# Kernel optimization log

Measured on AMD Instinct MI355X. Metric: run time of the kernel, lower is better.

Reference implementation:

```python
import jax, jax.numpy as jnp
import numpy as np

N_U = 8192  # users (rows of adj)
N_I = 8192  # items (cols of adj)
D_IN = 2048
D_H = 2048


def setup_inputs() -> dict:
    key = jax.random.key(0)
    k1, k2, k3, k4, k5 = jax.random.split(key, 5)
    input = jax.random.normal(k1, (N_U + N_I, D_IN), dtype=jnp.float32)
    adj = jax.random.uniform(k2, (N_U, N_I), dtype=jnp.float32)
    degree = jax.random.uniform(k3, (N_U + N_I,), dtype=jnp.float32)
    # Linear params (torch Linear: y = x @ W.T + b), xavier-normal-ish init
    W = jax.random.normal(k4, (D_H, D_IN), dtype=jnp.float32) * (2.0 / (D_IN + D_H)) ** 0.5
    b = jax.random.normal(k5, (D_H,), dtype=jnp.float32) * 0.01
    return {"input": input, "adj": adj, "degree": degree, "W": W, "b": b}


def reference(input, adj, degree, W, b):
    # Original builds block adjacency B = [[0, A], [A^T, 0]], then
    # output = diag(degree) @ B @ (dropout(input) @ W^T + b).
    # dropout p=0 (eval) -> identity. We avoid materializing B: the block
    # structure means user rows aggregate item supports and vice versa.
    n_u = adj.shape[0]
    support = input @ W.T + b                      # [N_u+N_i, D_h]
    sup_u, sup_i = support[:n_u], support[n_u:]
    out_u = degree[:n_u, None] * (adj @ sup_i)     # [N_u, D_h]
    out_i = degree[n_u:, None] * (adj.T @ sup_u)   # [N_i, D_h]
    return jnp.concatenate([out_u, out_i], axis=0)
```

## Files before the change

### kernel.cpp

```cpp
#include <hip/hip_runtime.h>
#include <hip/hip_bf16.h>


typedef __bf16 bf16;
typedef bf16 bf16x4 __attribute__((ext_vector_type(4)));
typedef bf16 bf16x8 __attribute__((ext_vector_type(8)));
typedef float f32x4 __attribute__((ext_vector_type(4)));

#define AS1 __attribute__((address_space(1)))
#define AS3 __attribute__((address_space(3)))

__global__ __launch_bounds__(256) void k_cvt(const float* __restrict__ src,
                                             bf16* __restrict__ dst) {
  long i = ((long)blockIdx.x * 256 + threadIdx.x) * 4;
  float4 v = *(const float4*)(src + i);
  bf16x4 o;
  o.x = (bf16)v.x; o.y = (bf16)v.y; o.z = (bf16)v.z; o.w = (bf16)v.w;
  *(bf16x4*)(dst + i) = o;
}

__global__ __launch_bounds__(256) void k_transpose_cvt(const float* __restrict__ src,
                                                       bf16* __restrict__ dst, int n) {
  __shared__ float tile[64][65];
  const int bx = blockIdx.x * 64;
  const int by = blockIdx.y * 64;
  const int tx = threadIdx.x & 15, ty = threadIdx.x >> 4;
#pragma unroll
  for (int p = 0; p < 4; ++p) {
    float4 v = *(const float4*)(src + (long)(by + p * 16 + ty) * n + bx + tx * 4);
    tile[p * 16 + ty][tx * 4 + 0] = v.x;
    tile[p * 16 + ty][tx * 4 + 1] = v.y;
    tile[p * 16 + ty][tx * 4 + 2] = v.z;
    tile[p * 16 + ty][tx * 4 + 3] = v.w;
  }
  __syncthreads();
#pragma unroll
  for (int p = 0; p < 4; ++p) {
    bf16x4 o;
    o.x = (bf16)tile[tx * 4 + 0][p * 16 + ty];
    o.y = (bf16)tile[tx * 4 + 1][p * 16 + ty];
    o.z = (bf16)tile[tx * 4 + 2][p * 16 + ty];
    o.w = (bf16)tile[tx * 4 + 3][p * 16 + ty];
    *(bf16x4*)(dst + (long)(bx + p * 16 + ty) * n + by + tx * 4) = o;
  }
}

template <bool OUT_BF16>
__global__ __launch_bounds__(256) void k_gemm_nt(
    const bf16* __restrict__ A, const bf16* __restrict__ B, void* __restrict__ Cout,
    int K, int lda, int ldb, int ldc,
    const float* __restrict__ rowscale, const float* __restrict__ rowbias) {
  constexpr int BK = 64;
  __shared__ __align__(16) bf16 As[128 * BK];
  __shared__ __align__(16) bf16 Bs[128 * BK];
  const int tid = threadIdx.x;
  const int wave = tid >> 6, lane = tid & 63;
  const int quad = lane >> 4, l16 = lane & 15;
  const int bm = blockIdx.y * 128, bn = blockIdx.x * 128;
  const bf16* Ab = A + (long)bm * lda;
  const bf16* Bb = B + (long)bn * ldb;
  f32x4 acc[4][4] = {};
  const int mrow = (wave & 1) * 64 + l16;
  const int ncol = (wave >> 1) * 64 + l16;
  const int xm = l16 & 7;

  for (int k0 = 0; k0 < K; k0 += BK) {
    __syncthreads();
#pragma unroll
    for (int it = 0; it < 4; ++it) {
      const int c = it * 256 + tid;
      const int row = c >> 3;
      const int kc = ((c & 7) ^ (row & 7)) * 8;
      __builtin_amdgcn_global_load_lds((AS1 void*)(Ab + row * lda + k0 + kc),
                                       (AS3 void*)(As + c * 8), 16, 0, 0);
      __builtin_amdgcn_global_load_lds((AS1 void*)(Bb + row * ldb + k0 + kc),
                                       (AS3 void*)(Bs + c * 8), 16, 0, 0);
    }
    __syncthreads();
#pragma unroll
    for (int ks = 0; ks < 2; ++ks) {
      const int jl = ks * 4 + quad;
      bf16x8 af[4], bfr[4];
#pragma unroll
      for (int i = 0; i < 4; ++i)
        af[i] = *(const bf16x8*)(As + (mrow + i * 16) * BK + ((jl ^ xm) << 3));
#pragma unroll
      for (int j = 0; j < 4; ++j)
        bfr[j] = *(const bf16x8*)(Bs + (ncol + j * 16) * BK + ((jl ^ xm) << 3));
#pragma unroll
      for (int i = 0; i < 4; ++i)
#pragma unroll
        for (int j = 0; j < 4; ++j)
          acc[i][j] = __builtin_amdgcn_mfma_f32_16x16x32_bf16(af[i], bfr[j], acc[i][j], 0, 0, 0);
    }
  }

#pragma unroll
  for (int i = 0; i < 4; ++i) {
    const int r0 = bm + (wave & 1) * 64 + i * 16 + quad * 4;
    float sc[4], bi[4];
#pragma unroll
    for (int r = 0; r < 4; ++r) {
      sc[r] = rowscale ? rowscale[r0 + r] : 1.0f;
      bi[r] = rowbias ? rowbias[r0 + r] : 0.0f;
    }
#pragma unroll
    for (int j = 0; j < 4; ++j) {
      const int col = bn + (wave >> 1) * 64 + j * 16 + l16;
#pragma unroll
      for (int r = 0; r < 4; ++r) {
        float v = acc[i][j][r] * sc[r] + bi[r];
        long idx = (long)(r0 + r) * ldc + col;
        if (OUT_BF16) ((bf16*)Cout)[idx] = (bf16)v;
        else          ((float*)Cout)[idx] = v;
      }
    }
  }
}

extern "C" void kernel_launch(void* const* d_in, const int* in_sizes, int n_in,
                              void* d_out, int out_size, void* d_ws, size_t ws_size,
                              hipStream_t stream) {
  const float* input  = (const float*)d_in[0];
  const float* adj    = (const float*)d_in[1];
  const float* degree = (const float*)d_in[2];
  const float* W      = (const float*)d_in[3];
  const float* b      = (const float*)d_in[4];
  float* out = (float*)d_out;

  char* ws = (char*)d_ws;
  bf16* supT   = (bf16*)(ws);
  bf16* in_bf  = (bf16*)(ws + (64ULL  << 20));
  bf16* W_bf   = (bf16*)(ws + (128ULL << 20));
  bf16* adj_bf = (bf16*)(ws + (64ULL  << 20));
  bf16* adjT   = (bf16*)(ws + (192ULL << 20));

  k_cvt<<<(16384 * 2048 / 4) / 256, 256, 0, stream>>>(input, in_bf);
  k_cvt<<<(2048 * 2048 / 4) / 256, 256, 0, stream>>>(W, W_bf);

  k_gemm_nt<true><<<dim3(16384 / 128, 2048 / 128), 256, 0, stream>>>(
      W_bf, in_bf, supT, 2048, 2048, 2048, 16384, nullptr, b);

  k_cvt<<<(8192 * 8192 / 4) / 256, 256, 0, stream>>>(adj, adj_bf);
  k_transpose_cvt<<<dim3(128, 128), 256, 0, stream>>>(adj, adjT, 8192);

  k_gemm_nt<false><<<dim3(2048 / 128, 8192 / 128), 256, 0, stream>>>(
      adj_bf, supT + 8192, out, 8192, 8192, 16384, 2048, degree, nullptr);

  k_gemm_nt<false><<<dim3(2048 / 128, 8192 / 128), 256, 0, stream>>>(
      adjT, supT, out + 8192LL * 2048, 8192, 8192, 16384, 2048, degree + 8192, nullptr);
}
```

Baseline: 1.421 ms.

## Use 256x256 double-buffered 8-wave GEMM and fuse adj convert with transpose

Replaces the 128x128 single-buffered GEMM with a 256x256-tile, 512-thread kernel. It double-buffers LDS and splits each K-step into four MFMA phases, interleaving the next tile's global-to-LDS loads with explicit waitcnt/barrier scheduling and setprio. It also merges the adj bf16 conversion and the transpose into one kernel, so adj is read from HBM once instead of twice. The larger tiles raise arithmetic intensity and overlap loads with compute, but LDS use per block grows to 128KB and the grid gets fewer blocks, which may limit occupancy.

```diff
diff --git a/kernel.cpp b/kernel.cpp
--- a/kernel.cpp
+++ b/kernel.cpp
@@ -19,19 +19,24 @@
   *(bf16x4*)(dst + i) = o;
 }
 
-__global__ __launch_bounds__(256) void k_transpose_cvt(const float* __restrict__ src,
-                                                       bf16* __restrict__ dst, int n) {
+__global__ __launch_bounds__(256) void k_adj_cvt(const float* __restrict__ src,
+                                                 bf16* __restrict__ dst,
+                                                 bf16* __restrict__ dstT, int n) {
   __shared__ float tile[64][65];
   const int bx = blockIdx.x * 64;
   const int by = blockIdx.y * 64;
   const int tx = threadIdx.x & 15, ty = threadIdx.x >> 4;
 #pragma unroll
   for (int p = 0; p < 4; ++p) {
-    float4 v = *(const float4*)(src + (long)(by + p * 16 + ty) * n + bx + tx * 4);
+    const long r = by + p * 16 + ty;
+    float4 v = *(const float4*)(src + r * n + bx + tx * 4);
     tile[p * 16 + ty][tx * 4 + 0] = v.x;
     tile[p * 16 + ty][tx * 4 + 1] = v.y;
     tile[p * 16 + ty][tx * 4 + 2] = v.z;
     tile[p * 16 + ty][tx * 4 + 3] = v.w;
+    bf16x4 o;
+    o.x = (bf16)v.x; o.y = (bf16)v.y; o.z = (bf16)v.z; o.w = (bf16)v.w;
+    *(bf16x4*)(dst + r * n + bx + tx * 4) = o;
   }
   __syncthreads();
 #pragma unroll
@@ -41,63 +46,148 @@
     o.y = (bf16)tile[tx * 4 + 1][p * 16 + ty];
     o.z = (bf16)tile[tx * 4 + 2][p * 16 + ty];
     o.w = (bf16)tile[tx * 4 + 3][p * 16 + ty];
-    *(bf16x4*)(dst + (long)(bx + p * 16 + ty) * n + by + tx * 4) = o;
-  }
+    *(bf16x4*)(dstT + (long)(bx + p * 16 + ty) * n + by + tx * 4) = o;
+  }
+}
+
+__device__ __forceinline__ void stage_a(const bf16* Ab, bf16* lds, int lda, int k0,
+                                        int g, int tid) {
+#pragma unroll
+  for (int it = 0; it < 2; ++it) {
+    const int u = it * 512 + tid;
+    const int row = ((u >> 9) << 7) + (g << 6) + ((u >> 3) & 63);
+    const int kc = (((u & 7) ^ (row & 7)) << 3);
+    const int c = ((u >> 9) << 10) + (g << 9) + (u & 511);
+    __builtin_amdgcn_global_load_lds((const AS1 void*)(Ab + (long)row * lda + k0 + kc),
+                                     (AS3 void*)(lds + c * 8), 16, 0, 0);
+  }
+}
+
+__device__ __forceinline__ void stage_b(const bf16* Bb, bf16* lds, int ldb, int k0,
+                                        int g, int tid) {
+#pragma unroll
+  for (int it = 0; it < 2; ++it) {
+    const int u = it * 512 + tid;
+    const int r = (g << 7) + (u >> 3);
+    const int p = (((u >> 8) & 3) << 6) + (g << 5) + ((u >> 3) & 31);
+    const int kc = (((u & 7) ^ (r & 7)) << 3);
+    __builtin_amdgcn_global_load_lds((const AS1 void*)(Bb + (long)p * ldb + k0 + kc),
+                                     (AS3 void*)(lds + ((g << 10) + u) * 8), 16, 0, 0);
+  }
+}
+
+template <int MH, int NH>
+__device__ __forceinline__ void mfma_phase(f32x4 (&acc)[8][4],
+                                           const bf16x8 (&af)[4][2],
+                                           const bf16x8 (&bfr)[2][2][2]) {
+  __builtin_amdgcn_s_setprio(1);
+#pragma unroll
+  for (int i = 0; i < 4; ++i)
+#pragma unroll
+    for (int j = 0; j < 2; ++j)
+#pragma unroll
+      for (int ks = 0; ks < 2; ++ks)
+        acc[MH * 4 + i][NH * 2 + j] = __builtin_amdgcn_mfma_f32_16x16x32_bf16(
+            af[i][ks], bfr[NH][j][ks], acc[MH * 4 + i][NH * 2 + j], 0, 0, 0);
+  __builtin_amdgcn_s_setprio(0);
 }
 
 template <bool OUT_BF16>
-__global__ __launch_bounds__(256) void k_gemm_nt(
+__global__ __launch_bounds__(512, 2) void k_gemm_nt_8p(
     const bf16* __restrict__ A, const bf16* __restrict__ B, void* __restrict__ Cout,
     int K, int lda, int ldb, int ldc,
     const float* __restrict__ rowscale, const float* __restrict__ rowbias) {
-  constexpr int BK = 64;
-  __shared__ __align__(16) bf16 As[128 * BK];
-  __shared__ __align__(16) bf16 Bs[128 * BK];
+  __shared__ __align__(16) bf16 As[2][256 * 64];
+  __shared__ __align__(16) bf16 Bs[2][256 * 64];
   const int tid = threadIdx.x;
   const int wave = tid >> 6, lane = tid & 63;
   const int quad = lane >> 4, l16 = lane & 15;
-  const int bm = blockIdx.y * 128, bn = blockIdx.x * 128;
+  const int wm = wave >> 2, wn = wave & 3;
+  const int xm = l16 & 7;
+  const int bm = blockIdx.y * 256, bn = blockIdx.x * 256;
   const bf16* Ab = A + (long)bm * lda;
   const bf16* Bb = B + (long)bn * ldb;
-  f32x4 acc[4][4] = {};
-  const int mrow = (wave & 1) * 64 + l16;
-  const int ncol = (wave >> 1) * 64 + l16;
-  const int xm = l16 & 7;
-
-  for (int k0 = 0; k0 < K; k0 += BK) {
-    __syncthreads();
-#pragma unroll
-    for (int it = 0; it < 4; ++it) {
-      const int c = it * 256 + tid;
-      const int row = c >> 3;
-      const int kc = ((c & 7) ^ (row & 7)) * 8;
-      __builtin_amdgcn_global_load_lds((AS1 void*)(Ab + row * lda + k0 + kc),
-                                       (AS3 void*)(As + c * 8), 16, 0, 0);
-      __builtin_amdgcn_global_load_lds((AS1 void*)(Bb + row * ldb + k0 + kc),
-                                       (AS3 void*)(Bs + c * 8), 16, 0, 0);
-    }
-    __syncthreads();
-#pragma unroll
-    for (int ks = 0; ks < 2; ++ks) {
-      const int jl = ks * 4 + quad;
-      bf16x8 af[4], bfr[4];
-#pragma unroll
-      for (int i = 0; i < 4; ++i)
-        af[i] = *(const bf16x8*)(As + (mrow + i * 16) * BK + ((jl ^ xm) << 3));
-#pragma unroll
-      for (int j = 0; j < 4; ++j)
-        bfr[j] = *(const bf16x8*)(Bs + (ncol + j * 16) * BK + ((jl ^ xm) << 3));
-#pragma unroll
-      for (int i = 0; i < 4; ++i)
-#pragma unroll
-        for (int j = 0; j < 4; ++j)
-          acc[i][j] = __builtin_amdgcn_mfma_f32_16x16x32_bf16(af[i], bfr[j], acc[i][j], 0, 0, 0);
-    }
-  }
-
-#pragma unroll
-  for (int i = 0; i < 4; ++i) {
-    const int r0 = bm + (wave & 1) * 64 + i * 16 + quad * 4;
+
+  f32x4 acc[8][4] = {};
+  bf16x8 af[4][2], bfr[2][2][2];
+
+  stage_a(Ab, As[0], lda, 0, 0, tid);
+  stage_b(Bb, Bs[0], ldb, 0, 0, tid);
+  stage_a(Ab, As[0], lda, 0, 1, tid);
+  stage_b(Bb, Bs[0], ldb, 0, 1, tid);
+  asm volatile("s_waitcnt vmcnt(4)" ::: "memory");
+  __builtin_amdgcn_s_barrier();
+
+  const int nt = K >> 6;
+  for (int t = 0; t < nt; ++t) {
+    const int cur = t & 1, nx = cur ^ 1;
+    const int k1 = (t + 1) << 6;
+    const bool pre = (t + 1) < nt;
+    const bf16* Ac = As[cur];
+    const bf16* Bc = Bs[cur];
+
+#pragma unroll
+    for (int i = 0; i < 4; ++i)
+#pragma unroll
+      for (int ks = 0; ks < 2; ++ks)
+        af[i][ks] = *(const bf16x8*)(Ac + (wm * 128 + i * 16 + l16) * 64 +
+                                     ((((ks << 2) + quad) ^ xm) << 3));
+#pragma unroll
+    for (int j = 0; j < 2; ++j)
+#pragma unroll
+      for (int ks = 0; ks < 2; ++ks)
+        bfr[0][j][ks] = *(const bf16x8*)(Bc + (wn * 32 + j * 16 + l16) * 64 +
+                                         ((((ks << 2) + quad) ^ xm) << 3));
+    if (pre) {
+      stage_a(Ab, As[nx], lda, k1, 0, tid);
+      stage_b(Bb, Bs[nx], ldb, k1, 0, tid);
+    }
+    __builtin_amdgcn_s_barrier();
+    asm volatile("s_waitcnt lgkmcnt(0)" ::: "memory");
+    __builtin_amdgcn_sched_barrier(0);
+    mfma_phase<0, 0>(acc, af, bfr);
+    if (pre) asm volatile("s_waitcnt vmcnt(4)" ::: "memory");
+    else     asm volatile("s_waitcnt vmcnt(0)" ::: "memory");
+    __builtin_amdgcn_s_barrier();
+
+#pragma unroll
+    for (int j = 0; j < 2; ++j)
+#pragma unroll
+      for (int ks = 0; ks < 2; ++ks)
+        bfr[1][j][ks] = *(const bf16x8*)(Bc + (128 + wn * 32 + j * 16 + l16) * 64 +
+                                         ((((ks << 2) + quad) ^ xm) << 3));
+    if (pre) {
+      stage_a(Ab, As[nx], lda, k1, 1, tid);
+      stage_b(Bb, Bs[nx], ldb, k1, 1, tid);
+    }
+    __builtin_amdgcn_s_barrier();
+    asm volatile("s_waitcnt lgkmcnt(0)" ::: "memory");
+    __builtin_amdgcn_sched_barrier(0);
+    mfma_phase<0, 1>(acc, af, bfr);
+    __builtin_amdgcn_s_barrier();
+
+#pragma unroll
+    for (int i = 0; i < 4; ++i)
+#pragma unroll
+      for (int ks = 0; ks < 2; ++ks)
+        af[i][ks] = *(const bf16x8*)(Ac + (wm * 128 + 64 + i * 16 + l16) * 64 +
+                                     ((((ks << 2) + quad) ^ xm) << 3));
+    __builtin_amdgcn_s_barrier();
+    asm volatile("s_waitcnt lgkmcnt(0)" ::: "memory");
+    __builtin_amdgcn_sched_barrier(0);
+    mfma_phase<1, 0>(acc, af, bfr);
+    __builtin_amdgcn_s_barrier();
+
+    mfma_phase<1, 1>(acc, af, bfr);
+    if (pre) {
+      asm volatile("s_waitcnt vmcnt(4)" ::: "memory");
+      __builtin_amdgcn_s_barrier();
+    }
+  }
+
+#pragma unroll
+  for (int mi = 0; mi < 8; ++mi) {
+    const int r0 = bm + wm * 128 + mi * 16 + quad * 4;
     float sc[4], bi[4];
 #pragma unroll
     for (int r = 0; r < 4; ++r) {
@@ -106,10 +196,10 @@
     }
 #pragma unroll
     for (int j = 0; j < 4; ++j) {
-      const int col = bn + (wave >> 1) * 64 + j * 16 + l16;
+      const int col = bn + wn * 64 + j * 16 + l16;
 #pragma unroll
       for (int r = 0; r < 4; ++r) {
-        float v = acc[i][j][r] * sc[r] + bi[r];
+        float v = acc[mi][j][r] * sc[r] + bi[r];
         long idx = (long)(r0 + r) * ldc + col;
         if (OUT_BF16) ((bf16*)Cout)[idx] = (bf16)v;
         else          ((float*)Cout)[idx] = v;
@@ -138,15 +228,14 @@
   k_cvt<<<(16384 * 2048 / 4) / 256, 256, 0, stream>>>(input, in_bf);
   k_cvt<<<(2048 * 2048 / 4) / 256, 256, 0, stream>>>(W, W_bf);
 
-  k_gemm_nt<true><<<dim3(16384 / 128, 2048 / 128), 256, 0, stream>>>(
+  k_gemm_nt_8p<true><<<dim3(16384 / 256, 2048 / 256), 512, 0, stream>>>(
       W_bf, in_bf, supT, 2048, 2048, 2048, 16384, nullptr, b);
 
-  k_cvt<<<(8192 * 8192 / 4) / 256, 256, 0, stream>>>(adj, adj_bf);
-  k_transpose_cvt<<<dim3(128, 128), 256, 0, stream>>>(adj, adjT, 8192);
-
-  k_gemm_nt<false><<<dim3(2048 / 128, 8192 / 128), 256, 0, stream>>>(
+  k_adj_cvt<<<dim3(128, 128), 256, 0, stream>>>(adj, adj_bf, adjT, 8192);
+
+  k_gemm_nt_8p<false><<<dim3(2048 / 256, 8192 / 256), 512, 0, stream>>>(
       adj_bf, supT + 8192, out, 8192, 8192, 16384, 2048, degree, nullptr);
 
-  k_gemm_nt<false><<<dim3(2048 / 128, 8192 / 128), 256, 0, stream>>>(
+  k_gemm_nt_8p<false><<<dim3(2048 / 256, 8192 / 256), 512, 0, stream>>>(
       adjT, supT, out + 8192LL * 2048, 8192, 8192, 16384, 2048, degree + 8192, nullptr);
 }
```

Result: faster. 1.250 ms (-12.0%).

## Replace GEMM with double-buffered 256x256 pipelined MFMA kernel and fuse adj conversions

Applied to the files above, without the earlier changes.

Swaps the simple 128x128 single-buffered GEMM for a 256x256-tile, 512-thread kernel. It double-buffers LDS and interleaves async global-to-LDS staging of the next K tile with MFMA phases, using explicit vmcnt waits, barriers and setprio. It also fuses the plain bf16 conversion of adj into the transpose kernel, so adj is read from HBM once instead of twice. Risks include heavy register pressure from 32 accumulators per thread, 128KB of LDS per block limiting occupancy, and fewer blocks per GEMM launch.

```diff
diff --git a/kernel.cpp b/kernel.cpp
--- a/kernel.cpp
+++ b/kernel.cpp
@@ -19,19 +19,24 @@
   *(bf16x4*)(dst + i) = o;
 }
 
-__global__ __launch_bounds__(256) void k_transpose_cvt(const float* __restrict__ src,
-                                                       bf16* __restrict__ dst, int n) {
+__global__ __launch_bounds__(256) void k_adj_cvt(const float* __restrict__ src,
+                                                 bf16* __restrict__ dst,
+                                                 bf16* __restrict__ dstT, int n) {
   __shared__ float tile[64][65];
   const int bx = blockIdx.x * 64;
   const int by = blockIdx.y * 64;
   const int tx = threadIdx.x & 15, ty = threadIdx.x >> 4;
 #pragma unroll
   for (int p = 0; p < 4; ++p) {
-    float4 v = *(const float4*)(src + (long)(by + p * 16 + ty) * n + bx + tx * 4);
+    const long r = by + p * 16 + ty;
+    float4 v = *(const float4*)(src + r * n + bx + tx * 4);
     tile[p * 16 + ty][tx * 4 + 0] = v.x;
     tile[p * 16 + ty][tx * 4 + 1] = v.y;
     tile[p * 16 + ty][tx * 4 + 2] = v.z;
     tile[p * 16 + ty][tx * 4 + 3] = v.w;
+    bf16x4 o;
+    o.x = (bf16)v.x; o.y = (bf16)v.y; o.z = (bf16)v.z; o.w = (bf16)v.w;
+    *(bf16x4*)(dst + r * n + bx + tx * 4) = o;
   }
   __syncthreads();
 #pragma unroll
@@ -41,63 +46,133 @@
     o.y = (bf16)tile[tx * 4 + 1][p * 16 + ty];
     o.z = (bf16)tile[tx * 4 + 2][p * 16 + ty];
     o.w = (bf16)tile[tx * 4 + 3][p * 16 + ty];
-    *(bf16x4*)(dst + (long)(bx + p * 16 + ty) * n + by + tx * 4) = o;
-  }
-}
+    *(bf16x4*)(dstT + (long)(bx + p * 16 + ty) * n + by + tx * 4) = o;
+  }
+}
+
+
+#define VM_WAIT4() asm volatile("s_waitcnt vmcnt(4)" ::: "memory")
+#define VM_WAIT0() asm volatile("s_waitcnt vmcnt(0)" ::: "memory")
+#define BARRIER() do { asm volatile("" ::: "memory"); \
+                       __builtin_amdgcn_s_barrier(); \
+                       asm volatile("" ::: "memory"); } while (0)
+
+#define READ_AF(dst, base, mh) \
+  _Pragma("unroll") for (int i = 0; i < 4; ++i) { \
+    dst[i][0] = *(const bf16x8*)((base) + arow0 + (mh) * 4096 + i * 1024 + sw0); \
+    dst[i][1] = *(const bf16x8*)((base) + arow0 + (mh) * 4096 + i * 1024 + sw1); \
+  }
+
+#define READ_BF(dst, base, nh) \
+  _Pragma("unroll") for (int j = 0; j < 2; ++j) { \
+    dst[j][0] = *(const bf16x8*)((base) + brow0 + (nh) * 8192 + j * 1024 + sw0); \
+    dst[j][1] = *(const bf16x8*)((base) + brow0 + (nh) * 8192 + j * 1024 + sw1); \
+  }
+
+#define MFMA_PH(mh, nh, afx, bfx) \
+  __builtin_amdgcn_s_setprio(1); \
+  _Pragma("unroll") for (int i = 0; i < 4; ++i) \
+  _Pragma("unroll") for (int j = 0; j < 2; ++j) \
+  _Pragma("unroll") for (int ks = 0; ks < 2; ++ks) \
+    acc[(mh) * 4 + i][(nh) * 2 + j] = __builtin_amdgcn_mfma_f32_16x16x32_bf16( \
+        afx[i][ks], bfx[j][ks], acc[(mh) * 4 + i][(nh) * 2 + j], 0, 0, 0); \
+  __builtin_amdgcn_s_setprio(0);
+
+#define STAGE_ALL(DA, DB, k0) do { \
+  _Pragma("unroll") for (int g = 0; g < 2; ++g) { \
+    _Pragma("unroll") for (int it = 0; it < 2; ++it) { \
+      __builtin_amdgcn_global_load_lds((const AS1 void*)(Ab + aoff[g * 2 + it] + (k0)), \
+                                       (AS3 void*)((DA) + alc[g * 2 + it]), 16, 0, 0); \
+      __builtin_amdgcn_global_load_lds((const AS1 void*)(Bb + boff[g * 2 + it] + (k0)), \
+                                       (AS3 void*)((DB) + blc[g * 2 + it]), 16, 0, 0); \
+    } \
+    __builtin_amdgcn_sched_barrier(0); \
+  } \
+} while (0)
+
+#define TILE(t, CURA, CURB, NXA, NXB, af0, bfr0, af0n, bfr0n) do { \
+  const bool pre = (t) + 1 < nt; \
+   \
+  READ_BF(bf1, CURB, 1); \
+  if (pre) STAGE_ALL(NXA, NXB, ((t) + 1) << 6); \
+  __builtin_amdgcn_sched_barrier(0); \
+  MFMA_PH(0, 0, af0, bfr0); \
+   \
+  READ_AF(af1, CURA, 1); \
+  __builtin_amdgcn_sched_barrier(0); \
+  MFMA_PH(0, 1, af0, bf1); \
+  if (pre) { VM_WAIT4(); BARRIER(); }  \
+   \
+  if (pre) { READ_BF(bfr0n, NXB, 0); } \
+  __builtin_amdgcn_sched_barrier(0); \
+  MFMA_PH(1, 0, af1, bfr0); \
+   \
+  if (pre) { READ_AF(af0n, NXA, 0); } \
+  __builtin_amdgcn_sched_barrier(0); \
+  MFMA_PH(1, 1, af1, bf1); \
+  if (pre) { VM_WAIT0(); BARRIER(); }  \
+} while (0)
 
 template <bool OUT_BF16>
-__global__ __launch_bounds__(256) void k_gemm_nt(
+__global__ __launch_bounds__(512, 2) void k_gemm_nt_pipe(
     const bf16* __restrict__ A, const bf16* __restrict__ B, void* __restrict__ Cout,
     int K, int lda, int ldb, int ldc,
     const float* __restrict__ rowscale, const float* __restrict__ rowbias) {
-  constexpr int BK = 64;
-  __shared__ __align__(16) bf16 As[128 * BK];
-  __shared__ __align__(16) bf16 Bs[128 * BK];
+  __shared__ __align__(16) bf16 As[2][256 * 64];
+  __shared__ __align__(16) bf16 Bs[2][256 * 64];
   const int tid = threadIdx.x;
   const int wave = tid >> 6, lane = tid & 63;
   const int quad = lane >> 4, l16 = lane & 15;
-  const int bm = blockIdx.y * 128, bn = blockIdx.x * 128;
+  const int wm = wave >> 2, wn = wave & 3;
+  const int xm = l16 & 7;
+  const int bm = blockIdx.y * 256, bn = blockIdx.x * 256;
   const bf16* Ab = A + (long)bm * lda;
   const bf16* Bb = B + (long)bn * ldb;
-  f32x4 acc[4][4] = {};
-  const int mrow = (wave & 1) * 64 + l16;
-  const int ncol = (wave >> 1) * 64 + l16;
-  const int xm = l16 & 7;
-
-  for (int k0 = 0; k0 < K; k0 += BK) {
-    __syncthreads();
-#pragma unroll
-    for (int it = 0; it < 4; ++it) {
-      const int c = it * 256 + tid;
-      const int row = c >> 3;
-      const int kc = ((c & 7) ^ (row & 7)) * 8;
-      __builtin_amdgcn_global_load_lds((AS1 void*)(Ab + row * lda + k0 + kc),
-                                       (AS3 void*)(As + c * 8), 16, 0, 0);
-      __builtin_amdgcn_global_load_lds((AS1 void*)(Bb + row * ldb + k0 + kc),
-                                       (AS3 void*)(Bs + c * 8), 16, 0, 0);
+
+  const int arow0 = wm * 8192 + l16 * 64;
+  const int brow0 = wn * 2048 + l16 * 64;
+  const int sw0 = ((0 + quad) ^ xm) << 3;
+  const int sw1 = ((4 + quad) ^ xm) << 3;
+
+  int aoff[4], alc[4], boff[4], blc[4];
+#pragma unroll
+  for (int g = 0; g < 2; ++g)
+#pragma unroll
+    for (int it = 0; it < 2; ++it) {
+      const int u = it * 512 + tid;
+      const int arow = ((u >> 9) << 7) + (g << 6) + ((u >> 3) & 63);
+      aoff[g * 2 + it] = arow * lda + ((((u & 7) ^ (arow & 7)) << 3));
+      alc[g * 2 + it] = (((u >> 9) << 10) + (g << 9) + (u & 511)) * 8;
+      const int br = (g << 7) + (u >> 3);
+      const int bp = (((u >> 8) & 3) << 6) + (g << 5) + ((u >> 3) & 31);
+      boff[g * 2 + it] = bp * ldb + ((((u & 7) ^ (br & 7)) << 3));
+      blc[g * 2 + it] = ((g << 10) + u) * 8;
     }
-    __syncthreads();
-#pragma unroll
-    for (int ks = 0; ks < 2; ++ks) {
-      const int jl = ks * 4 + quad;
-      bf16x8 af[4], bfr[4];
-#pragma unroll
-      for (int i = 0; i < 4; ++i)
-        af[i] = *(const bf16x8*)(As + (mrow + i * 16) * BK + ((jl ^ xm) << 3));
-#pragma unroll
-      for (int j = 0; j < 4; ++j)
-        bfr[j] = *(const bf16x8*)(Bs + (ncol + j * 16) * BK + ((jl ^ xm) << 3));
-#pragma unroll
-      for (int i = 0; i < 4; ++i)
-#pragma unroll
-        for (int j = 0; j < 4; ++j)
-          acc[i][j] = __builtin_amdgcn_mfma_f32_16x16x32_bf16(af[i], bfr[j], acc[i][j], 0, 0, 0);
-    }
-  }
-
-#pragma unroll
-  for (int i = 0; i < 4; ++i) {
-    const int r0 = bm + (wave & 1) * 64 + i * 16 + quad * 4;
+
+  f32x4 acc[8][4] = {};
+  bf16x8 afP[4][2], afQ[4][2], af1[4][2];
+  bf16x8 bfP[2][2], bfQ[2][2], bf1[2][2];
+
+  bf16* const A0 = &As[0][0];
+  bf16* const A1s = &As[1][0];
+  bf16* const B0 = &Bs[0][0];
+  bf16* const B1s = &Bs[1][0];
+
+  STAGE_ALL(A0, B0, 0);
+  VM_WAIT0();
+  BARRIER();
+  READ_AF(afP, A0, 0);
+  READ_BF(bfP, B0, 0);
+
+  const int nt = K >> 6;
+  for (int t = 0; t < nt; t += 2) {
+    TILE(t,     A0,  B0,  A1s, B1s, afP, bfP, afQ, bfQ);
+    TILE(t + 1, A1s, B1s, A0,  B0,  afQ, bfQ, afP, bfP);
+  }
+
+#pragma unroll
+  for (int mi = 0; mi < 8; ++mi) {
+    const int r0 = bm + wm * 128 + mi * 16 + quad * 4;
     float sc[4], bi[4];
 #pragma unroll
     for (int r = 0; r < 4; ++r) {
@@ -106,10 +181,10 @@
     }
 #pragma unroll
     for (int j = 0; j < 4; ++j) {
-      const int col = bn + (wave >> 1) * 64 + j * 16 + l16;
+      const int col = bn + wn * 64 + j * 16 + l16;
 #pragma unroll
       for (int r = 0; r < 4; ++r) {
-        float v = acc[i][j][r] * sc[r] + bi[r];
+        float v = acc[mi][j][r] * sc[r] + bi[r];
         long idx = (long)(r0 + r) * ldc + col;
         if (OUT_BF16) ((bf16*)Cout)[idx] = (bf16)v;
         else          ((float*)Cout)[idx] = v;
@@ -138,15 +213,14 @@
   k_cvt<<<(16384 * 2048 / 4) / 256, 256, 0, stream>>>(input, in_bf);
   k_cvt<<<(2048 * 2048 / 4) / 256, 256, 0, stream>>>(W, W_bf);
 
-  k_gemm_nt<true><<<dim3(16384 / 128, 2048 / 128), 256, 0, stream>>>(
+  k_gemm_nt_pipe<true><<<dim3(16384 / 256, 2048 / 256), 512, 0, stream>>>(
       W_bf, in_bf, supT, 2048, 2048, 2048, 16384, nullptr, b);
 
-  k_cvt<<<(8192 * 8192 / 4) / 256, 256, 0, stream>>>(adj, adj_bf);
-  k_transpose_cvt<<<dim3(128, 128), 256, 0, stream>>>(adj, adjT, 8192);
-
-  k_gemm_nt<false><<<dim3(2048 / 128, 8192 / 128), 256, 0, stream>>>(
+  k_adj_cvt<<<dim3(128, 128), 256, 0, stream>>>(adj, adj_bf, adjT, 8192);
+
+  k_gemm_nt_pipe<false><<<dim3(2048 / 256, 8192 / 256), 512, 0, stream>>>(
       adj_bf, supT + 8192, out, 8192, 8192, 16384, 2048, degree, nullptr);
 
-  k_gemm_nt<false><<<dim3(2048 / 128, 8192 / 128), 256, 0, stream>>>(
+  k_gemm_nt_pipe<false><<<dim3(2048 / 256, 8192 / 256), 512, 0, stream>>>(
       adjT, supT, out + 8192LL * 2048, 8192, 8192, 16384, 2048, degree + 8192, nullptr);
 }
```

Result: slower. 3.691 ms (+159.8%).
